# Kernel tuning notes

Hardware: AMD Instinct MI355X
Metric: run time of the kernel (lower is better)

Reference implementation:

```python
import jax, jax.numpy as jnp
import numpy as np

EMBED_DIM = 1024
NUM_HEADS = 16
HEAD_DIM = EMBED_DIM // NUM_HEADS
HIDDEN_DIM = 4096


def layer_norm(x, gamma, beta, eps=1e-5):
    mu = jnp.mean(x, axis=-1, keepdims=True)
    var = jnp.var(x, axis=-1, keepdims=True)
    return (x - mu) * jax.lax.rsqrt(var + eps) * gamma + beta


def setup_inputs() -> dict:
    key = jax.random.key(0)
    ks = jax.random.split(key, 12)
    D, H3, F = EMBED_DIM, 3 * EMBED_DIM, HIDDEN_DIM
    s_d = 1.0 / np.sqrt(D)
    s_f = 1.0 / np.sqrt(F)
    return {
        "x": jax.random.normal(ks[0], (2, 2048, D), dtype=jnp.float32),
        "w_qkv": jax.random.uniform(ks[1], (D, H3), jnp.float32, -s_d, s_d),
        "b_qkv": jax.random.uniform(ks[2], (H3,), jnp.float32, -s_d, s_d),
        "w_out": jax.random.uniform(ks[3], (D, D), jnp.float32, -s_d, s_d),
        "b_out": jax.random.uniform(ks[4], (D,), jnp.float32, -s_d, s_d),
        "w_fc1": jax.random.uniform(ks[5], (D, F), jnp.float32, -s_d, s_d),
        "b_fc1": jax.random.uniform(ks[6], (F,), jnp.float32, -s_d, s_d),
        "w_fc2": jax.random.uniform(ks[7], (F, D), jnp.float32, -s_f, s_f),
        "b_fc2": jax.random.uniform(ks[8], (D,), jnp.float32, -s_f, s_f),
        "ln1_g": jnp.ones((D,), jnp.float32),
        "ln1_b": jnp.zeros((D,), jnp.float32),
        "ln2_g": jnp.ones((D,), jnp.float32),
        "ln2_b": jnp.zeros((D,), jnp.float32),
    }


def reference(x, w_qkv, b_qkv, w_out, b_out, w_fc1, b_fc1, w_fc2, b_fc2,
              ln1_g, ln1_b, ln2_g, ln2_b):
    B, N, D = x.shape
    H, Hd = NUM_HEADS, HEAD_DIM

    # --- attention branch (pre-LN) ---
    h = layer_norm(x, ln1_g, ln1_b)
    qkv = h @ w_qkv + b_qkv                              # [B,N,3D]
    qkv = qkv.reshape(B, N, 3, H, Hd).transpose(2, 0, 3, 1, 4)  # [3,B,H,N,Hd]
    q, k, v = qkv[0], qkv[1], qkv[2]
    scores = jnp.einsum("bhnd,bhmd->bhnm", q, k) * (Hd ** -0.5)  # [B,H,N,N]
    attn = jax.nn.softmax(scores, axis=-1)
    out = jnp.einsum("bhnm,bhmd->bhnd", attn, v)         # [B,H,N,Hd]
    out = out.transpose(0, 2, 1, 3).reshape(B, N, D)
    x = x + (out @ w_out + b_out)

    # --- FFN branch (pre-LN) ---
    h = layer_norm(x, ln2_g, ln2_b)
    h = jax.nn.gelu(h @ w_fc1 + b_fc1, approximate=False)  # torch F.gelu default (erf)
    x = x + (h @ w_fc2 + b_fc2)
    return x
```

## Files before the change

kernel.cpp:

```cpp
#include <hip/hip_runtime.h>
#include <hip/hip_bf16.h>

#define D_ 1024
#define F_ 4096
#define NH 16
#define HD 64
#define SEQ 2048
#define TOK 4096

typedef short bf16x8 __attribute__((ext_vector_type(8)));
typedef float f32x4 __attribute__((ext_vector_type(4)));
typedef unsigned int u32x4 __attribute__((ext_vector_type(4)));

static __device__ __forceinline__ f32x4 mfma16(bf16x8 a, bf16x8 b, f32x4 c) {
  return __builtin_amdgcn_mfma_f32_16x16x32_bf16(a, b, c, 0, 0, 0);
}

static __device__ __forceinline__ unsigned short f2bf(float f) {
  union { float f; unsigned int u; } a; a.f = f;
  unsigned int u = a.u;
  u += 0x7fffu + ((u >> 16) & 1u);
  return (unsigned short)(u >> 16);
}

static __device__ __forceinline__ unsigned int cvtpk(float lo, float hi) {
  unsigned int r;
  asm("v_cvt_pk_bf16_f32 %0, %1, %2" : "=v"(r) : "v"(lo), "v"(hi));
  return r;
}

#define AS1 __attribute__((address_space(1)))
#define AS3 __attribute__((address_space(3)))
static __device__ __forceinline__ void gld16(const void* g, void* l) {
  __builtin_amdgcn_global_load_lds((const AS1 unsigned int*)(uintptr_t)(g),
                                   (AS3 unsigned int*)(uintptr_t)(l), 16, 0, 0);
}

#define WAITBAR0()                                       \
  do {                                                   \
    asm volatile("s_waitcnt vmcnt(0)" ::: "memory");     \
    __builtin_amdgcn_s_barrier();                        \
    __builtin_amdgcn_sched_barrier(0);                   \
  } while (0)

__global__ void transpose_all(const float* __restrict__ wqkv, const float* __restrict__ wout,
                              const float* __restrict__ wfc1, const float* __restrict__ wfc2,
                              unsigned short* __restrict__ oqkv, unsigned short* __restrict__ oout,
                              unsigned short* __restrict__ ofc1, unsigned short* __restrict__ ofc2) {
  __shared__ float tile[32][33];
  int idx = blockIdx.x;
  const float* in;
  unsigned short* out;
  int K, N;
  if (idx < 3072)      { in = wqkv; out = oqkv; K = 1024; N = 3072; }
  else if (idx < 4096) { in = wout; out = oout; K = 1024; N = 1024; idx -= 3072; }
  else if (idx < 8192) { in = wfc1; out = ofc1; K = 1024; N = 4096; idx -= 4096; }
  else                 { in = wfc2; out = ofc2; K = 4096; N = 1024; idx -= 8192; }
  int nt = N >> 5;
  int n0 = (idx % nt) * 32, k0 = (idx / nt) * 32;
  int tx = threadIdx.x, ty = threadIdx.y;
#pragma unroll
  for (int i = 0; i < 32; i += 8)
    tile[ty + i][tx] = in[(size_t)(k0 + ty + i) * N + n0 + tx];
  __syncthreads();
#pragma unroll
  for (int i = 0; i < 32; i += 8)
    out[(size_t)(n0 + ty + i) * K + k0 + tx] = f2bf(tile[tx][ty + i]);
}

__global__ __launch_bounds__(256) void layernorm_bf16(const float* __restrict__ x,
                                                      const float* __restrict__ g,
                                                      const float* __restrict__ bta,
                                                      unsigned short* __restrict__ out) {
  int wv = threadIdx.x >> 6, lane = threadIdx.x & 63;
  int row = blockIdx.x * 4 + wv;
  const float4* xr = (const float4*)(x + (size_t)row * D_);
  float4 v[4];
  float s = 0.f, ss = 0.f;
#pragma unroll
  for (int i = 0; i < 4; i++) {
    v[i] = xr[i * 64 + lane];
    s += v[i].x + v[i].y + v[i].z + v[i].w;
    ss += v[i].x * v[i].x + v[i].y * v[i].y + v[i].z * v[i].z + v[i].w * v[i].w;
  }
#pragma unroll
  for (int off = 32; off >= 1; off >>= 1) {
    s += __shfl_xor(s, off);
    ss += __shfl_xor(ss, off);
  }
  float mu = s * (1.0f / D_);
  float var = ss * (1.0f / D_) - mu * mu;
  float r = rsqrtf(var + 1e-5f);
#pragma unroll
  for (int i = 0; i < 4; i++) {
    int col = i * 256 + lane * 4;
    unsigned short ob[4];
    ob[0] = f2bf((v[i].x - mu) * r * g[col + 0] + bta[col + 0]);
    ob[1] = f2bf((v[i].y - mu) * r * g[col + 1] + bta[col + 1]);
    ob[2] = f2bf((v[i].z - mu) * r * g[col + 2] + bta[col + 2]);
    ob[3] = f2bf((v[i].w - mu) * r * g[col + 3] + bta[col + 3]);
    *(ushort4*)(out + (size_t)row * D_ + col) = *(ushort4*)ob;
  }
}

template <int MODE, int NBUF, int TN, int SWZ>
__global__ __launch_bounds__(256, (NBUF == 2 ? 4 : 3)) void gemm_bt(
    const unsigned short* __restrict__ A, const unsigned short* __restrict__ Bt,
    const float* __restrict__ bias, const float* __restrict__ resid,
    void* __restrict__ outp, int M, int N, int K) {
  constexpr int BSZ = TN * 64;
  constexpr int NI = TN / 32;
  __shared__ __align__(16) char lds_all[NBUF * (8192 + BSZ)];
  char* const a_lds = lds_all;
  char* const b_lds = lds_all + NBUF * 8192;
  const int t = threadIdx.x;
  const int lane = t & 63, w = t >> 6;
  const int g = lane >> 4, lr = lane & 15;
  const int wm = (w >> 1) * 64, wn = (w & 1) * (TN / 2);
  int m0, n0;
  if constexpr (SWZ) {
    const int gx = gridDim.x;
    const int lid = blockIdx.y * gx + blockIdx.x;
    const int chunk = (gx * gridDim.y) >> 3;
    const int sidx = (lid & 7) * chunk + (lid >> 3);
    m0 = (sidx / gx) * 128;
    n0 = (sidx % gx) * TN;
  } else {
    m0 = blockIdx.y * 128;
    n0 = blockIdx.x * TN;
  }
  const int nIter = K / 32;

  const int mac0 = t >> 3;
  const int v0 = ((t & 7) ^ (mac0 & 7)) << 4;
  const int cc0 = v0 & 63;
  const int growA = mac0 + ((v0 >> 6) << 6);
  const int growB = mac0 + ((v0 >> 6) << (TN == 128 ? 6 : 5));
  const char* srcA0 = (const char*)A + ((size_t)(m0 + growA) * K) * 2 + cc0;
  const char* srcA1 = srcA0 + (size_t)32 * K * 2;
  const char* srcB0 = (const char*)Bt + ((size_t)(n0 + growB) * K) * 2 + cc0;
  const char* srcB1 = srcB0 + (size_t)32 * K * 2;

  const int rsw = (lr & 7) << 4;
  const int rdA = lr * 128 + (((wm & 64) + g * 16) ^ rsw);
  const int rdB = lr * 128 + ((((TN == 128) ? (wn & 64) : ((wn & 32) * 2)) + g * 16) ^ rsw);

#define STAGE(IT, BUF)                                                    \
  do {                                                                    \
    size_t kb = (size_t)(IT) * 64;                                        \
    gld16(srcA0 + kb, a_lds + (BUF) * 8192 + t * 16);                     \
    gld16(srcA1 + kb, a_lds + (BUF) * 8192 + 4096 + t * 16);              \
    gld16(srcB0 + kb, b_lds + (BUF) * BSZ + t * 16);                      \
    if constexpr (TN == 128)                                              \
      gld16(srcB1 + kb, b_lds + (BUF) * BSZ + 4096 + t * 16);             \
  } while (0)

#define GSTEP(BUF)                                                           \
  do {                                                                       \
    bf16x8 af[4], bfr[NI];                                                   \
    _Pragma("unroll") for (int mi = 0; mi < 4; mi++)                         \
        af[mi] = *(const bf16x8*)(a_lds + (BUF) * 8192 + rdA + mi * 2048);   \
    _Pragma("unroll") for (int ni = 0; ni < NI; ni++)                        \
        bfr[ni] = *(const bf16x8*)(b_lds + (BUF) * BSZ + rdB + ni * 2048);   \
    _Pragma("unroll") for (int mi = 0; mi < 4; mi++)                         \
        _Pragma("unroll") for (int ni = 0; ni < NI; ni++)                    \
            acc[mi][ni] = mfma16(af[mi], bfr[ni], acc[mi][ni]);              \
  } while (0)

#define WAITBAR_OLD()                                                     \
  do {                                                                    \
    if constexpr (TN == 128)                                              \
      asm volatile("s_waitcnt vmcnt(4)" ::: "memory");                    \
    else                                                                  \
      asm volatile("s_waitcnt vmcnt(3)" ::: "memory");                    \
    __builtin_amdgcn_s_barrier();                                         \
    __builtin_amdgcn_sched_barrier(0);                                    \
  } while (0)

  f32x4 acc[4][NI] = {};
  if constexpr (NBUF == 2) {
    STAGE(0, 0);
    int cur = 0;
#pragma unroll 1
    for (int it = 0; it < nIter; ++it) {
      WAITBAR0();
      if (it + 1 < nIter) STAGE(it + 1, cur ^ 1);
      GSTEP(cur);
      cur ^= 1;
    }
  } else {
    STAGE(0, 0);
    STAGE(1, 1);
    int b0 = 0, b1 = 1, b2 = 2;
#pragma unroll 1
    for (int it = 0; it < nIter - 1; ++it) {
      WAITBAR_OLD();
      if (it + 2 < nIter) STAGE(it + 2, b2);
      GSTEP(b0);
      int tmp = b0; b0 = b1; b1 = b2; b2 = tmp;
    }
    WAITBAR0();
    GSTEP(b0);
  }
#undef STAGE
#undef GSTEP
#undef WAITBAR_OLD

  if (MODE == 0) {
    const int whichB = n0 >> 10;
    if (whichB == 2) {
      __syncthreads();
#pragma unroll
      for (int mi = 0; mi < 4; mi++) {
        int colbase = wm + mi * 16 + g * 4;
        int off = colbase & 63;
        int cpos = (off & 35) | ((off & 4) << 1) | ((off & 8) << 1) | ((off & 16) >> 2);
        int nplb = ((colbase & 64) + cpos) * 2;
#pragma unroll
        for (int ni = 0; ni < NI; ni++) {
          int rl = wn + ni * 16 + lr;
          float bia = bias[n0 + rl];
          unsigned short v4[4];
#pragma unroll
          for (int j = 0; j < 4; j++) v4[j] = f2bf(acc[mi][ni][j] + bia);
          int byt = rl * 256 + (nplb ^ ((rl & 7) << 4));
          *(unsigned long long*)(lds_all + byt) = *(const unsigned long long*)v4;
        }
      }
      __syncthreads();
      int r = t >> 1, half = t & 1;
      int hh = ((n0 & 1023) >> 6) + (r >> 6);
      int dd = r & 63;
      int bb = m0 >> 11;
      char* dst = (char*)outp +
                  2 * ((size_t)2 * TOK * D_ +
                       ((size_t)(bb * NH + hh) * HD + dd) * SEQ + (m0 & 2047) + half * 64);
#pragma unroll
      for (int c = 0; c < 8; c++) {
        int src = r * 256 + ((half * 128 + c * 16) ^ ((r & 7) << 4));
        *(int4*)(dst + c * 16) = *(const int4*)(lds_all + src);
      }
    } else {
#pragma unroll
      for (int mi = 0; mi < 4; mi++) {
#pragma unroll
        for (int ni = 0; ni < NI; ni++) {
#pragma unroll
          for (int j = 0; j < 4; j++) {
            int row = m0 + wm + mi * 16 + g * 4 + j;
            int col = n0 + wn + ni * 16 + lr;
            float val = acc[mi][ni][j] + bias[col];
            int cc = col & 1023;
            int hh = cc >> 6, dd = cc & 63;
            int bb = row >> 11, nn = row & 2047;
            if (whichB == 0) val *= 0.18033688011112042f;
            ((unsigned short*)outp)[(size_t)whichB * (TOK * D_) +
                                    (((size_t)(bb * NH + hh) * SEQ + nn) << 6) + dd] =
                f2bf(val);
          }
        }
      }
    }
    return;
  }

#pragma unroll
  for (int mi = 0; mi < 4; mi++) {
#pragma unroll
    for (int ni = 0; ni < NI; ni++) {
#pragma unroll
      for (int j = 0; j < 4; j++) {
        int row = m0 + wm + mi * 16 + g * 4 + j;
        int col = n0 + wn + ni * 16 + lr;
        float val = acc[mi][ni][j];
        if (MODE == 2) {
          val += bias[col];
          val = 0.5f * val * (1.0f + erff(val * 0.70710678118f));
          ((unsigned short*)outp)[(size_t)row * N + col] = f2bf(val);
        } else if (MODE == 5) {
          val += bias[col] + resid[(size_t)row * N + col];
          ((float*)outp)[(size_t)row * N + col] = val;
        }
      }
    }
  }
}

__global__ __launch_bounds__(256, 4) void attn_kernel(const unsigned short* __restrict__ q,
                                                      const unsigned short* __restrict__ k,
                                                      const unsigned short* __restrict__ vT,
                                                      unsigned short* __restrict__ ao) {
  __shared__ __align__(16) char ldsb[32768];
  const int t = threadIdx.x, lane = t & 63, w = t >> 6;
  const int g = lane >> 4, lr = lane & 15;
  const int bid = (blockIdx.x & 7) * 128 + (blockIdx.x >> 3);
  const int qt = bid & 31, bh = bid >> 5;
  const int bb = bh >> 4, hh = bh & 15;

  const unsigned short* qp = q + ((size_t)bh * SEQ + qt * 64 + w * 16) * HD;
  bf16x8 qf0 = *(const bf16x8*)(qp + lr * HD + g * 8);
  bf16x8 qf1 = *(const bf16x8*)(qp + lr * HD + 32 + g * 8);

  f32x4 oacc[4] = {};
  f32x4 spv = {0.f, 0.f, 0.f, 0.f};

  const int srow = t >> 3, sc = (t & 7) << 4;
  const int ssw = sc ^ ((srow & 7) << 4);
  const char* kgl = (const char*)(k + (size_t)bh * SEQ * HD) + srow * 128 + ssw;
  const char* vgl = (const char*)(vT + (size_t)bh * HD * SEQ) + (size_t)srow * 4096 + ssw;
  char* kdst = ldsb + w * 1024;
  char* vdst = ldsb + 16384 + w * 1024;

  const int rsw = (lr & 7) << 4;
  const char* r0 = ldsb + lr * 128 + ((g * 16) ^ rsw);
  const char* r1 = ldsb + lr * 128 + ((64 + g * 16) ^ rsw);

#define ISSUE(BUF)                                   \
  do {                                               \
    gld16(kgl, kdst + (BUF) * 8192);                 \
    gld16(kgl + 4096, kdst + (BUF) * 8192 + 4096);   \
    gld16(vgl, vdst + (BUF) * 8192);                 \
    gld16(vgl + 131072, vdst + (BUF) * 8192 + 4096); \
    kgl += 8192;                                     \
    vgl += 128;                                      \
  } while (0)

#define COMPUTE(BUF)                                                                     \
  do {                                                                                   \
    f32x4 sT[4];                                                                         \
    __builtin_amdgcn_s_setprio(1);                                                       \
    _Pragma("unroll") for (int sb = 0; sb < 4; ++sb) {                                   \
      bf16x8 kf0 = *(const bf16x8*)(r0 + (BUF) * 8192 + sb * 2048);                      \
      bf16x8 kf1 = *(const bf16x8*)(r1 + (BUF) * 8192 + sb * 2048);                      \
      f32x4 zz = {};                                                                     \
      zz = mfma16(kf0, qf0, zz);                                                         \
      sT[sb] = mfma16(kf1, qf1, zz);                                                     \
    }                                                                                    \
    __builtin_amdgcn_s_setprio(0);                                                       \
    float p[4][4];                                                                       \
    _Pragma("unroll") for (int sb = 0; sb < 4; ++sb) _Pragma("unroll")                   \
        for (int jr = 0; jr < 4; ++jr) {                                                 \
      p[sb][jr] = exp2f(sT[sb][jr]);                                                     \
      spv[jr] += p[sb][jr];                                                              \
    }                                                                                    \
    u32x4 pA[2];                                                                         \
    _Pragma("unroll") for (int kk = 0; kk < 2; ++kk) pA[kk] =                            \
        (u32x4){cvtpk(p[2 * kk][0], p[2 * kk][1]), cvtpk(p[2 * kk][2], p[2 * kk][3]),    \
                cvtpk(p[2 * kk + 1][0], p[2 * kk + 1][1]),                               \
                cvtpk(p[2 * kk + 1][2], p[2 * kk + 1][3])};                              \
    __builtin_amdgcn_s_setprio(1);                                                       \
    _Pragma("unroll") for (int vb = 0; vb < 4; ++vb) {                                   \
      bf16x8 v0 = *(const bf16x8*)(r0 + 16384 + (BUF) * 8192 + vb * 2048);               \
      bf16x8 v1 = *(const bf16x8*)(r1 + 16384 + (BUF) * 8192 + vb * 2048);               \
      oacc[vb] = mfma16(__builtin_bit_cast(bf16x8, pA[0]), v0, oacc[vb]);                \
      oacc[vb] = mfma16(__builtin_bit_cast(bf16x8, pA[1]), v1, oacc[vb]);                \
    }                                                                                    \
    __builtin_amdgcn_s_setprio(0);                                                       \
  } while (0)

  ISSUE(0);

  int staged = 1;
#pragma unroll 1
  for (int i2 = 0; i2 < SEQ / 128; ++i2) {
    WAITBAR0();
    if (staged < SEQ / 64) { ISSUE(1); ++staged; }
    COMPUTE(0);
    WAITBAR0();
    if (staged < SEQ / 64) { ISSUE(0); ++staged; }
    COMPUTE(1);
  }
#undef ISSUE
#undef COMPUTE

  float sp = (spv[0] + spv[1]) + (spv[2] + spv[3]);
  sp += __shfl_xor(sp, 16);
  sp += __shfl_xor(sp, 32);

#pragma unroll
  for (int jj = 0; jj < 4; ++jj) {
    float li = 1.0f / __shfl(sp, g * 4 + jj);
    int nrow = qt * 64 + w * 16 + g * 4 + jj;
#pragma unroll
    for (int vb = 0; vb < 4; ++vb)
      ao[((size_t)bb * SEQ + nrow) * D_ + hh * HD + vb * 16 + lr] = f2bf(oacc[vb][jj] * li);
  }
}

extern "C" void kernel_launch(void* const* d_in, const int* in_sizes, int n_in,
                              void* d_out, int out_size, void* d_ws, size_t ws_size,
                              hipStream_t stream) {
  const float* x     = (const float*)d_in[0];
  const float* w_qkv = (const float*)d_in[1];
  const float* b_qkv = (const float*)d_in[2];
  const float* w_out = (const float*)d_in[3];
  const float* b_out = (const float*)d_in[4];
  const float* w_fc1 = (const float*)d_in[5];
  const float* b_fc1 = (const float*)d_in[6];
  const float* w_fc2 = (const float*)d_in[7];
  const float* b_fc2 = (const float*)d_in[8];
  const float* ln1_g = (const float*)d_in[9];
  const float* ln1_b = (const float*)d_in[10];
  const float* ln2_g = (const float*)d_in[11];
  const float* ln2_b = (const float*)d_in[12];
  float* out = (float*)d_out;

  char* ws = (char*)d_ws;
  unsigned short* wqkvT = (unsigned short*)(ws);
  unsigned short* woutT = (unsigned short*)(ws + 6291456);
  unsigned short* wfc1T = (unsigned short*)(ws + 8388608);
  unsigned short* wfc2T = (unsigned short*)(ws + 16777216);
  unsigned short* h     = (unsigned short*)(ws + 25165824);
  unsigned short* qkv   = (unsigned short*)(ws + 33554432);
  unsigned short* ao    = (unsigned short*)(ws + 58720256);
  float*          x1    = (float*)(ws + 67108864);
  unsigned short* hg    = (unsigned short*)(ws + 83886080);

  transpose_all<<<12288, dim3(32, 8), 0, stream>>>(w_qkv, w_out, w_fc1, w_fc2,
                                                   wqkvT, woutT, wfc1T, wfc2T);

  layernorm_bf16<<<TOK / 4, 256, 0, stream>>>(x, ln1_g, ln1_b, h);
  gemm_bt<0, 3, 128, 0><<<dim3(24, 32), 256, 0, stream>>>(h, wqkvT, b_qkv, nullptr, qkv,
                                                          TOK, 3072, 1024);
  attn_kernel<<<1024, 256, 0, stream>>>(qkv, qkv + (size_t)TOK * D_, qkv + 2 * (size_t)TOK * D_,
                                        ao);
  gemm_bt<5, 3, 64, 0><<<dim3(16, 32), 256, 0, stream>>>(ao, woutT, b_out, x, x1,
                                                         TOK, 1024, 1024);
  layernorm_bf16<<<TOK / 4, 256, 0, stream>>>(x1, ln2_g, ln2_b, h);
  gemm_bt<2, 2, 128, 0><<<dim3(32, 32), 256, 0, stream>>>(h, wfc1T, b_fc1, nullptr, hg,
                                                          TOK, 4096, 1024);
  gemm_bt<5, 3, 64, 1><<<dim3(16, 32), 256, 0, stream>>>(hg, wfc2T, b_fc2, x1, out,
                                                         TOK, 1024, 4096);
}
```

Measured before the change: 237.2 us.

## Split-K the FC2 GEMM into two halves with a separate reduction pass

The FC2 GEMM (K=4096) now runs with a grid z-dimension of 2, so each block handles half of K. Slice 0 adds bias and residual and writes the output, slice 1 writes raw partials into a scratch buffer that reuses the transposed QKV weight region, and a new reduce_add kernel sums the two. This doubles the block count of the 512-block FC2 launch to fill the GPU better, at the cost of an extra 16MB float write, read and reduce pass plus one more launch. The launch-bound occupancy hint for TN=64 instantiations also rises from 3 to 4.

```diff
diff --git a/kernel.cpp b/kernel.cpp
--- a/kernel.cpp
+++ b/kernel.cpp
@@ -103,11 +103,21 @@
   }
 }
 
+__global__ __launch_bounds__(256) void reduce_add(float4* __restrict__ out,
+                                                  const float4* __restrict__ p1) {
+#pragma unroll
+  for (int j = 0; j < 4; ++j) {
+    int i = blockIdx.x * 1024 + j * 256 + threadIdx.x;
+    float4 o = out[i], a = p1[i];
+    out[i] = make_float4(o.x + a.x, o.y + a.y, o.z + a.z, o.w + a.w);
+  }
+}
+
 template <int MODE, int NBUF, int TN, int SWZ>
-__global__ __launch_bounds__(256, (NBUF == 2 ? 4 : 3)) void gemm_bt(
+__global__ __launch_bounds__(256, ((NBUF == 2 || TN == 64) ? 4 : 3)) void gemm_bt(
     const unsigned short* __restrict__ A, const unsigned short* __restrict__ Bt,
     const float* __restrict__ bias, const float* __restrict__ resid,
-    void* __restrict__ outp, int M, int N, int K) {
+    void* __restrict__ outp, float* __restrict__ p1, int M, int N, int K, int KSPL) {
   constexpr int BSZ = TN * 64;
   constexpr int NI = TN / 32;
   __shared__ __align__(16) char lds_all[NBUF * (8192 + BSZ)];
@@ -129,16 +139,18 @@
     m0 = blockIdx.y * 128;
     n0 = blockIdx.x * TN;
   }
-  const int nIter = K / 32;
+  const int z = blockIdx.z;
+  const int kt0 = z * KSPL;
+  const int nIter = KSPL / 32;
 
   const int mac0 = t >> 3;
   const int v0 = ((t & 7) ^ (mac0 & 7)) << 4;
   const int cc0 = v0 & 63;
   const int growA = mac0 + ((v0 >> 6) << 6);
   const int growB = mac0 + ((v0 >> 6) << (TN == 128 ? 6 : 5));
-  const char* srcA0 = (const char*)A + ((size_t)(m0 + growA) * K) * 2 + cc0;
+  const char* srcA0 = (const char*)A + ((size_t)(m0 + growA) * K + kt0) * 2 + cc0;
   const char* srcA1 = srcA0 + (size_t)32 * K * 2;
-  const char* srcB0 = (const char*)Bt + ((size_t)(n0 + growB) * K) * 2 + cc0;
+  const char* srcB0 = (const char*)Bt + ((size_t)(n0 + growB) * K + kt0) * 2 + cc0;
   const char* srcB1 = srcB0 + (size_t)32 * K * 2;
 
   const int rsw = (lr & 7) << 4;
@@ -278,8 +290,12 @@
           val = 0.5f * val * (1.0f + erff(val * 0.70710678118f));
           ((unsigned short*)outp)[(size_t)row * N + col] = f2bf(val);
         } else if (MODE == 5) {
-          val += bias[col] + resid[(size_t)row * N + col];
-          ((float*)outp)[(size_t)row * N + col] = val;
+          if (z == 0) {
+            val += bias[col] + resid[(size_t)row * N + col];
+            ((float*)outp)[(size_t)row * N + col] = val;
+          } else {
+            p1[(size_t)row * N + col] = val;
+          }
         }
       }
     }
@@ -415,20 +431,22 @@
   unsigned short* ao    = (unsigned short*)(ws + 58720256);
   float*          x1    = (float*)(ws + 67108864);
   unsigned short* hg    = (unsigned short*)(ws + 83886080);
+  float* p_fc1 = (float*)(ws);
 
   transpose_all<<<12288, dim3(32, 8), 0, stream>>>(w_qkv, w_out, w_fc1, w_fc2,
                                                    wqkvT, woutT, wfc1T, wfc2T);
 
   layernorm_bf16<<<TOK / 4, 256, 0, stream>>>(x, ln1_g, ln1_b, h);
   gemm_bt<0, 3, 128, 0><<<dim3(24, 32), 256, 0, stream>>>(h, wqkvT, b_qkv, nullptr, qkv,
-                                                          TOK, 3072, 1024);
+                                                          nullptr, TOK, 3072, 1024, 1024);
   attn_kernel<<<1024, 256, 0, stream>>>(qkv, qkv + (size_t)TOK * D_, qkv + 2 * (size_t)TOK * D_,
                                         ao);
   gemm_bt<5, 3, 64, 0><<<dim3(16, 32), 256, 0, stream>>>(ao, woutT, b_out, x, x1,
-                                                         TOK, 1024, 1024);
+                                                         nullptr, TOK, 1024, 1024, 1024);
   layernorm_bf16<<<TOK / 4, 256, 0, stream>>>(x1, ln2_g, ln2_b, h);
   gemm_bt<2, 2, 128, 0><<<dim3(32, 32), 256, 0, stream>>>(h, wfc1T, b_fc1, nullptr, hg,
-                                                          TOK, 4096, 1024);
-  gemm_bt<5, 3, 64, 1><<<dim3(16, 32), 256, 0, stream>>>(hg, wfc2T, b_fc2, x1, out,
-                                                         TOK, 1024, 4096);
-}
+                                                          nullptr, TOK, 4096, 1024, 1024);
+  gemm_bt<5, 3, 64, 1><<<dim3(16, 32, 2), 256, 0, stream>>>(hg, wfc2T, b_fc2, x1, out,
+                                                            p_fc1, TOK, 1024, 4096, 2048);
+  reduce_add<<<1024, 256, 0, stream>>>((float4*)out, (const float4*)p_fc1);
+}
```

After: 256.4 us. 1.08x slower.
